# Optimization experiments

Hardware: AMD Instinct MI355X
Metric: run time of the kernel (lower is better)

Reference implementation:

```python
import jax, jax.numpy as jnp
import numpy as np

DIM, H, DH, MLP, ADIM = 512, 8, 64, 2048, 256
B, T = 4, 2048
EPS = 1e-5


def setup_inputs() -> dict:
    key = jax.random.key(0)
    ks = jax.random.split(key, 10)
    s = 0.02
    inner = H * DH
    return {
        "x": jax.random.normal(ks[0], (B, T, DIM), jnp.float32),
        "action_emb": jax.random.normal(ks[1], (B, T, ADIM), jnp.float32),
        "causal_mask": jnp.tril(jnp.ones((T, T), dtype=bool)),
        "Wqkv": jax.random.normal(ks[2], (3 * inner, DIM), jnp.float32) * s,
        "Wout": jax.random.normal(ks[3], (DIM, inner), jnp.float32) * s,
        "bout": jnp.zeros((DIM,), jnp.float32),
        "W1": jax.random.normal(ks[4], (MLP, DIM), jnp.float32) * s,
        "b1": jnp.zeros((MLP,), jnp.float32),
        "W2": jax.random.normal(ks[5], (DIM, MLP), jnp.float32) * s,
        "b2": jnp.zeros((DIM,), jnp.float32),
        # adaLN is zero-init in the module; use small random so modulation is exercised
        "Wmod": jax.random.normal(ks[6], (6 * DIM, ADIM), jnp.float32) * s,
        "bmod": jnp.zeros((6 * DIM,), jnp.float32),
    }


def _layernorm(z):
    mu = jnp.mean(z, axis=-1, keepdims=True)
    var = jnp.var(z, axis=-1, keepdims=True)
    return (z - mu) * jax.lax.rsqrt(var + EPS)


def reference(x, action_emb, causal_mask, Wqkv, Wout, bout, W1, b1, W2, b2, Wmod, bmod):
    b, t, d = x.shape
    mod = jax.nn.silu(action_emb) @ Wmod.T + bmod            # (B,T,6*dim)
    shift1, scale1, gate1, shift2, scale2, gate2 = jnp.split(mod, 6, axis=-1)

    h = _layernorm(x) * (1.0 + scale1) + shift1
    qkv = (h @ Wqkv.T).reshape(b, t, 3, H, DH)
    q, k, v = qkv[:, :, 0], qkv[:, :, 1], qkv[:, :, 2]        # (B,T,H,DH)
    scores = jnp.einsum("bqhd,bkhd->bhqk", q, k) * (DH ** -0.5)
    scores = jnp.where(causal_mask, scores, -jnp.inf)
    attn = jax.nn.softmax(scores, axis=-1)                   # dropout=eval (identity)
    h = jnp.einsum("bhqk,bkhd->bqhd", attn, v).reshape(b, t, H * DH)
    h = h @ Wout.T + bout
    x = x + gate1 * h

    h = _layernorm(x) * (1.0 + scale2) + shift2
    h = jax.nn.gelu(h @ W1.T + b1, approximate=False) @ W2.T + b2
    return x + gate2 * h
```

## Files before the change

kernel.cpp:

```cpp
#include <hip/hip_runtime.h>
#include <math.h>
#include <stdint.h>

#define BB 4
#define TT 2048
#define NTOK 8192
#define DIMD 512
#define HH 8
#define DHH 64
#define MLPD 2048
#define ADIMD 256
#define MODD 3072
#define LNEPS 1e-5f
#define LOG2E_8 0.18033688011112042f
#define PBLK 4224

typedef short short8 __attribute__((ext_vector_type(8)));
typedef unsigned short ushort4v __attribute__((ext_vector_type(4)));
typedef __bf16 bf16x8 __attribute__((ext_vector_type(8)));
typedef float f32x4 __attribute__((ext_vector_type(4)));

static __device__ __forceinline__ unsigned short f2bf(float f) {
    union { float f; unsigned u; } v; v.f = f;
    unsigned r = v.u + 0x7fffu + ((v.u >> 16) & 1u);
    return (unsigned short)(r >> 16);
}
static __device__ __forceinline__ float bf2f(unsigned short u) {
    union { unsigned u; float f; } v; v.u = (unsigned)u << 16; return v.f;
}
static __device__ __forceinline__ unsigned pk2bf(float a, float b) {
    return (unsigned)f2bf(a) | ((unsigned)f2bf(b) << 16);
}

static __device__ __forceinline__ f32x4 mfma_bf16(short8 a, short8 b, f32x4 c) {
    return __builtin_amdgcn_mfma_f32_16x16x32_bf16(
        __builtin_bit_cast(bf16x8, a), __builtin_bit_cast(bf16x8, b), c, 0, 0, 0);
}

struct CvtArgs {
    const float* s[6];
    unsigned short* d[6];
    int cum[7];
};
__global__ __launch_bounds__(256) void cvt_all(CvtArgs a)
{
    const int i = blockIdx.x * 256 + threadIdx.x;
    if (i >= a.cum[6]) return;
    int seg = 0;
    #pragma unroll
    for (int k = 1; k < 6; k++) seg += (i >= a.cum[k]);
    const int off = i - a.cum[seg];
    float4 v = ((const float4*)a.s[seg])[off];
    if (seg == 5) {
        v.x = v.x / (1.f + __expf(-v.x));
        v.y = v.y / (1.f + __expf(-v.y));
        v.z = v.z / (1.f + __expf(-v.z));
        v.w = v.w / (1.f + __expf(-v.w));
    }
    uint2 o;
    o.x = pk2bf(v.x, v.y);
    o.y = pk2bf(v.z, v.w);
    ((uint2*)a.d[seg])[off] = o;
}

template<int EPI, int BN>
__global__ __launch_bounds__(256, (BN == 128 ? 3 : 4)) void gemm_bf16(
    const unsigned short* __restrict__ A, const unsigned short* __restrict__ Bw,
    const float* __restrict__ bias, const float* __restrict__ res,
    const unsigned short* __restrict__ mod,
    int M, int N, int K,
    void* __restrict__ Cv)
{
    constexpr int MT = (BN == 128) ? 4 : 2;
    constexpr int NPB = (BN == 128) ? 4 : 2;
    __shared__ unsigned short As[128 * 76];
    __shared__ unsigned short Bs[BN * 76];

    const int tid = threadIdx.x;
    const int w = tid >> 6, lane = tid & 63;
    const int quad = lane >> 4, l16 = lane & 15;
    const int wrow = (BN == 128) ? (w >> 1) * 64 : w * 32;
    const int wcol = (BN == 128) ? (w & 1) * 64 : 0;
    const int row0 = blockIdx.y * 128, col0 = blockIdx.x * BN;

    const int srow = tid >> 3;
    const int skc  = (tid & 7) * 8;

    f32x4 acc[MT][4];
    #pragma unroll
    for (int i = 0; i < MT; i++)
        #pragma unroll
        for (int j = 0; j < 4; j++) acc[i][j] = (f32x4){0.f, 0.f, 0.f, 0.f};

    short8 pA[4], pB[NPB];
    auto prefetch = [&](int k0) {
        #pragma unroll
        for (int p = 0; p < 4; p++)
            pA[p] = *(const short8*)&A[(size_t)(row0 + srow + p * 32) * K + k0 + skc];
        #pragma unroll
        for (int p = 0; p < NPB; p++)
            pB[p] = *(const short8*)&Bw[(size_t)(col0 + srow + p * 32) * K + k0 + skc];
    };
    auto stage = [&]() {
        #pragma unroll
        for (int p = 0; p < 4; p++)
            *(short8*)&As[(srow + p * 32) * 76 + skc] = pA[p];
        #pragma unroll
        for (int p = 0; p < NPB; p++)
            *(short8*)&Bs[(srow + p * 32) * 76 + skc] = pB[p];
    };

    prefetch(0);
    stage();
    __syncthreads();

    for (int k0 = 0; k0 < K; k0 += 64) {
        const bool more = (k0 + 64 < K);
        if (more) prefetch(k0 + 64);

        #pragma unroll
        for (int ks = 0; ks < 2; ks++) {
            short8 af[MT], bf[4];
            #pragma unroll
            for (int mt = 0; mt < MT; mt++)
                af[mt] = *(const short8*)&As[(wrow + mt * 16 + l16) * 76 + ks * 32 + quad * 8];
            #pragma unroll
            for (int nt = 0; nt < 4; nt++)
                bf[nt] = *(const short8*)&Bs[(wcol + nt * 16 + l16) * 76 + ks * 32 + quad * 8];
            #pragma unroll
            for (int nt = 0; nt < 4; nt++)
                #pragma unroll
                for (int mt = 0; mt < MT; mt++)
                    acc[mt][nt] = mfma_bf16(af[mt], bf[nt], acc[mt][nt]);
        }
        __syncthreads();
        if (more) stage();
        __syncthreads();
    }

    float* Cf = (float*)Cv;
    unsigned short* Cb = (unsigned short*)Cv;
    #pragma unroll
    for (int mt = 0; mt < MT; mt++) {
        #pragma unroll
        for (int r = 0; r < 4; r++) {
            const int row = row0 + wrow + mt * 16 + quad * 4 + r;
            #pragma unroll
            for (int nt = 0; nt < 4; nt++) {
                const int col = col0 + wcol + nt * 16 + l16;
                const size_t idx = (size_t)row * N + col;
                const float v = acc[mt][nt][r];
                if (EPI == 0) {
                    Cb[idx] = f2bf(v);
                } else if (EPI == 2) {
                    float t = v + bias[col];
                    Cb[idx] = f2bf(0.5f * t * (1.f + erff(t * 0.70710678118654752f)));
                } else if (EPI == 3) {
                    float t = v + bias[col];
                    Cf[idx] = res[idx] + bf2f(mod[(size_t)row * MODD + 1024 + col]) * t;
                } else if (EPI == 4) {
                    float t = v + bias[col];
                    Cf[idx] = Cf[idx] + bf2f(mod[(size_t)row * MODD + 2560 + col]) * t;
                } else if (EPI == 5) {
                    Cb[idx] = f2bf(v + bias[col]);
                }
            }
        }
    }
}

__global__ __launch_bounds__(256) void adaln_ln(
    const float* __restrict__ src, const unsigned short* __restrict__ mod,
    unsigned short* __restrict__ dst, int shift_off, int scale_off)
{
    const int n = blockIdx.x;
    const int tid = threadIdx.x;
    const float* xr = src + (size_t)n * DIMD;
    float v0 = xr[tid], v1 = xr[tid + 256];
    float s = v0 + v1;
    float q = v0 * v0 + v1 * v1;
    #pragma unroll
    for (int o = 32; o > 0; o >>= 1) {
        s += __shfl_down(s, o);
        q += __shfl_down(q, o);
    }
    __shared__ float sh[8];
    __shared__ float mu_sh, rs_sh;
    const int wid = tid >> 6, lane = tid & 63;
    if (lane == 0) { sh[wid] = s; sh[wid + 4] = q; }
    __syncthreads();
    if (tid == 0) {
        float S = sh[0] + sh[1] + sh[2] + sh[3];
        float Q = sh[4] + sh[5] + sh[6] + sh[7];
        float mu = S * (1.f / DIMD);
        float var = Q * (1.f / DIMD) - mu * mu;
        mu_sh = mu;
        rs_sh = rsqrtf(var + LNEPS);
    }
    __syncthreads();
    const float mu = mu_sh, rs = rs_sh;
    const unsigned short* mrow = mod + (size_t)n * MODD;
    const size_t o0 = (size_t)n * DIMD + tid;
    dst[o0]       = f2bf((v0 - mu) * rs * (1.f + bf2f(mrow[scale_off + tid]))       + bf2f(mrow[shift_off + tid]));
    dst[o0 + 256] = f2bf((v1 - mu) * rs * (1.f + bf2f(mrow[scale_off + tid + 256])) + bf2f(mrow[shift_off + tid + 256]));
}

__global__ __launch_bounds__(256, 4) void attn_mfma(
    const unsigned short* __restrict__ qkv, float* __restrict__ part)
{
    __shared__ unsigned short Kt[64][76];
    __shared__ unsigned short Vt[64][76];
    __shared__ unsigned short Ps[4][16][76];

    const int f = 79 - (int)blockIdx.x;
    int qi, ch;
    if (f < 8)       { qi = f;               ch = 0; }
    else if (f < 24) { const int g = f - 8;  qi = 8 + (g >> 1);  ch = g & 1; }
    else if (f < 48) { const int g = f - 24; qi = 16 + g / 3;    ch = g % 3; }
    else             { const int g = f - 48; qi = 24 + (g >> 2); ch = g & 3; }

    const int h = blockIdx.y, b = blockIdx.z;
    const int tid = threadIdx.x;
    const int w = tid >> 6;
    const int lane = tid & 63;
    const int quad = lane >> 4;
    const int l16 = lane & 15;

    const int qw = qi * 64 + w * 16;
    const size_t tokbase = (size_t)b * TT;

    short8 qf[2];
    {
        const unsigned short* qp = qkv + (tokbase + qw + l16) * 1536 + h * 64 + quad * 8;
        #pragma unroll
        for (int hd = 0; hd < 2; hd++) {
            short8 raw = *(const short8*)(qp + hd * 32);
            short8 fr;
            #pragma unroll
            for (int j = 0; j < 8; j++)
                fr[j] = (short)f2bf(bf2f((unsigned short)raw[j]) * LOG2E_8);
            qf[hd] = fr;
        }
    }

    f32x4 Oa[4];
    float mrun = -INFINITY, lrun = 0.f;
    #pragma unroll
    for (int mt = 0; mt < 4; mt++) Oa[mt] = (f32x4){0.f, 0.f, 0.f, 0.f};

    const int k0t = ch * 8;
    const int k1t = min(k0t + 8, qi + 1);
    const int vk0 = (tid & 31) * 2;
    const int vdb = (tid >> 5) * 8;

    short8 kpre[2], vpre[2];
    auto prefetchKV = [&](int kt) {
        const unsigned short* kb = qkv + (tokbase + (size_t)kt * 64) * 1536 + 512 + h * 64;
        #pragma unroll
        for (int it = 0; it < 2; it++) {
            const int i = tid + it * 256;
            kpre[it] = *(const short8*)(kb + (size_t)(i >> 3) * 1536 + (i & 7) * 8);
        }
        const unsigned short* vb = qkv + (tokbase + (size_t)kt * 64 + vk0) * 1536 + 1024 + h * 64 + vdb;
        vpre[0] = *(const short8*)vb;
        vpre[1] = *(const short8*)(vb + 1536);
    };
    auto storeKV = [&]() {
        #pragma unroll
        for (int it = 0; it < 2; it++) {
            const int i = tid + it * 256;
            *(short8*)&Kt[i >> 3][(i & 7) * 8] = kpre[it];
        }
        #pragma unroll
        for (int j = 0; j < 8; j++) {
            *(unsigned*)&Vt[vdb + j][vk0] =
                (unsigned)(unsigned short)vpre[0][j]
                | ((unsigned)(unsigned short)vpre[1][j] << 16);
        }
    };

    prefetchKV(k0t);
    storeKV();
    __syncthreads();

    for (int kt = k0t; kt < k1t; kt++) {
        const bool haveNext = (kt + 1 < k1t);
        if (haveNext) prefetchKV(kt + 1);

        f32x4 st[4];
        #pragma unroll
        for (int mk = 0; mk < 4; mk++) {
            const short8 a0 = *(const short8*)&Kt[mk * 16 + l16][quad * 8];
            const short8 a1 = *(const short8*)&Kt[mk * 16 + l16][32 + quad * 8];
            st[mk] = (f32x4){0.f, 0.f, 0.f, 0.f};
            st[mk] = mfma_bf16(a0, qf[0], st[mk]);
            st[mk] = mfma_bf16(a1, qf[1], st[mk]);
        }
        if (kt == qi) {
            const int qrel = w * 16 + l16;
            #pragma unroll
            for (int mk = 0; mk < 4; mk++)
                #pragma unroll
                for (int r = 0; r < 4; r++)
                    if (mk * 16 + quad * 4 + r > qrel) st[mk][r] = -INFINITY;
        }
        float tm = -INFINITY;
        #pragma unroll
        for (int mk = 0; mk < 4; mk++)
            #pragma unroll
            for (int r = 0; r < 4; r++) tm = fmaxf(tm, st[mk][r]);
        tm = fmaxf(tm, __shfl_xor(tm, 16));
        tm = fmaxf(tm, __shfl_xor(tm, 32));
        const float mn = fmaxf(mrun, tm);
        const float alpha = __builtin_amdgcn_exp2f(mrun - mn);
        mrun = mn;
        float ts = 0.f;
        #pragma unroll
        for (int mk = 0; mk < 4; mk++) {
            const float p0 = __builtin_amdgcn_exp2f(st[mk][0] - mn);
            const float p1 = __builtin_amdgcn_exp2f(st[mk][1] - mn);
            const float p2 = __builtin_amdgcn_exp2f(st[mk][2] - mn);
            const float p3 = __builtin_amdgcn_exp2f(st[mk][3] - mn);
            ts += (p0 + p1) + (p2 + p3);
            const unsigned long long pk =
                (unsigned long long)pk2bf(p0, p1)
                | ((unsigned long long)pk2bf(p2, p3) << 32);
            *(unsigned long long*)&Ps[w][l16][mk * 16 + quad * 4] = pk;
        }
        ts += __shfl_xor(ts, 16);
        ts += __shfl_xor(ts, 32);
        lrun = lrun * alpha + ts;
        #pragma unroll
        for (int mt = 0; mt < 4; mt++) Oa[mt] *= alpha;
        __threadfence_block();

        short8 pf[2];
        #pragma unroll
        for (int kc = 0; kc < 2; kc++)
            pf[kc] = *(const short8*)&Ps[w][l16][kc * 32 + quad * 8];
        #pragma unroll
        for (int mt = 0; mt < 4; mt++)
            #pragma unroll
            for (int kc = 0; kc < 2; kc++) {
                const short8 vf = *(const short8*)&Vt[mt * 16 + l16][kc * 32 + quad * 8];
                Oa[mt] = mfma_bf16(vf, pf[kc], Oa[mt]);
            }

        __syncthreads();
        if (haveNext) storeKV();
        __syncthreads();
    }

    float* pO = part + ((size_t)((b * HH + h) * 80 + f)) * PBLK;
    #pragma unroll
    for (int mt = 0; mt < 4; mt++)
        *(f32x4*)&pO[(w * 16 + l16) * 64 + mt * 16 + quad * 4] = Oa[mt];
    if (quad == 0) {
        pO[4096 + (w * 16 + l16) * 2]     = mrun;
        pO[4096 + (w * 16 + l16) * 2 + 1] = lrun;
    }
}

__global__ __launch_bounds__(256) void attn_combine(
    const float* __restrict__ part, unsigned short* __restrict__ outb)
{
    const int idx = blockIdx.x * 256 + threadIdx.x;
    const int d4 = idx & 15;
    const int h = (idx >> 4) & 7;
    const int tok = idx >> 7;
    const int t = tok & (TT - 1);
    const int b = tok >> 11;
    const int qi = t >> 6;
    const int nch = (qi >> 3) + 1;
    int cum;
    if (qi < 8)       cum = qi;
    else if (qi < 16) cum = 8 + ((qi - 8) << 1);
    else if (qi < 24) cum = 24 + (qi - 16) * 3;
    else              cum = 48 + ((qi - 24) << 2);
    const int qloc = t & 63;
    const float* base = part + ((size_t)((b * HH + h) * 80 + cum)) * PBLK;

    float M = -INFINITY;
    for (int c = 0; c < nch; c++)
        M = fmaxf(M, base[c * PBLK + 4096 + qloc * 2]);
    float L = 0.f, a0 = 0.f, a1 = 0.f, a2 = 0.f, a3 = 0.f;
    for (int c = 0; c < nch; c++) {
        const float m = base[c * PBLK + 4096 + qloc * 2];
        const float l = base[c * PBLK + 4097 + qloc * 2];
        const float sc = __builtin_amdgcn_exp2f(m - M);
        L += l * sc;
        const float4 o = *(const float4*)&base[c * PBLK + qloc * 64 + d4 * 4];
        a0 += sc * o.x; a1 += sc * o.y; a2 += sc * o.z; a3 += sc * o.w;
    }
    const float inv = 1.f / L;
    const unsigned long long pk =
        (unsigned long long)pk2bf(a0 * inv, a1 * inv)
        | ((unsigned long long)pk2bf(a2 * inv, a3 * inv) << 32);
    *(unsigned long long*)&outb[(size_t)tok * DIMD + h * 64 + d4 * 4] = pk;
}

extern "C" void kernel_launch(void* const* d_in, const int* in_sizes, int n_in,
                              void* d_out, int out_size, void* d_ws, size_t ws_size,
                              hipStream_t stream)
{
    (void)in_sizes; (void)n_in; (void)out_size; (void)ws_size;

    const float* x    = (const float*)d_in[0];
    const float* aemb = (const float*)d_in[1];
    const float* Wqkv = (const float*)d_in[3];
    const float* Wout = (const float*)d_in[4];
    const float* bout = (const float*)d_in[5];
    const float* W1   = (const float*)d_in[6];
    const float* b1   = (const float*)d_in[7];
    const float* W2   = (const float*)d_in[8];
    const float* b2   = (const float*)d_in[9];
    const float* Wmod = (const float*)d_in[10];
    const float* bmod = (const float*)d_in[11];

    float* out = (float*)d_out;

    char* p = (char*)d_ws;
    unsigned short* modw = (unsigned short*)p; p += (size_t)NTOK * MODD * 2;
    unsigned short* h12  = (unsigned short*)p; p += (size_t)NTOK * DIMD * 2;
    unsigned short* qkvb = (unsigned short*)p; p += (size_t)NTOK * 1536 * 2;
    unsigned short* attw = (unsigned short*)p; p += (size_t)NTOK * DIMD * 2;
    unsigned short* hid  = qkvb;
    unsigned short* sact = (unsigned short*)p; p += (size_t)NTOK * ADIMD * 2;
    unsigned short* wq = (unsigned short*)p;   p += (size_t)1536 * 512 * 2;
    unsigned short* wo = (unsigned short*)p;   p += (size_t)512 * 512 * 2;
    unsigned short* w1 = (unsigned short*)p;   p += (size_t)2048 * 512 * 2;
    unsigned short* w2 = (unsigned short*)p;   p += (size_t)512 * 2048 * 2;
    unsigned short* wm = (unsigned short*)p;   p += (size_t)3072 * 256 * 2;
    p = (char*)(((uintptr_t)p + 255) & ~(uintptr_t)255);
    float* part = (float*)p;

    CvtArgs ca;
    ca.s[0] = Wqkv; ca.d[0] = wq;
    ca.s[1] = Wout; ca.d[1] = wo;
    ca.s[2] = W1;   ca.d[2] = w1;
    ca.s[3] = W2;   ca.d[3] = w2;
    ca.s[4] = Wmod; ca.d[4] = wm;
    ca.s[5] = aemb; ca.d[5] = sact;
    const int n4s[6] = {1536 * 512 / 4, 512 * 512 / 4, 2048 * 512 / 4,
                        512 * 2048 / 4, 3072 * 256 / 4, NTOK * ADIMD / 4};
    ca.cum[0] = 0;
    for (int i = 0; i < 6; i++) ca.cum[i + 1] = ca.cum[i] + n4s[i];
    cvt_all<<<(ca.cum[6] + 255) / 256, 256, 0, stream>>>(ca);

    gemm_bf16<5, 128><<<dim3(MODD / 128, NTOK / 128), 256, 0, stream>>>(
        sact, wm, bmod, nullptr, nullptr, NTOK, MODD, ADIMD, modw);

    adaln_ln<<<NTOK, 256, 0, stream>>>(x, modw, h12, 0, 512);

    gemm_bf16<0, 128><<<dim3(1536 / 128, NTOK / 128), 256, 0, stream>>>(
        h12, wq, nullptr, nullptr, nullptr, NTOK, 1536, DIMD, qkvb);

    attn_mfma<<<dim3(80, HH, BB), 256, 0, stream>>>(qkvb, part);
    attn_combine<<<NTOK * HH * 16 / 256, 256, 0, stream>>>(part, attw);

    gemm_bf16<3, 64><<<dim3(DIMD / 64, NTOK / 128), 256, 0, stream>>>(
        attw, wo, bout, x, modw, NTOK, DIMD, DIMD, out);

    adaln_ln<<<NTOK, 256, 0, stream>>>(out, modw, h12, 1536, 2048);

    gemm_bf16<2, 128><<<dim3(MLPD / 128, NTOK / 128), 256, 0, stream>>>(
        h12, w1, b1, nullptr, nullptr, NTOK, MLPD, DIMD, hid);

    gemm_bf16<4, 64><<<dim3(DIMD / 64, NTOK / 128), 256, 0, stream>>>(
        hid, w2, b2, nullptr, modw, NTOK, DIMD, MLPD, out);
}
```

Measured before the change: 326.6 us.

## Transpose attention probabilities via shuffles and add lazy softmax rescaling

The attention kernel no longer stages the probability tile in shared memory. It redistributes the packed bf16 values across lanes with cross-lane shuffles, which removes the LDS round trip and the block fence. Online-softmax rescaling of the running sum and output accumulator is now skipped unless some lane's new max exceeds the running max by more than 8 (log2 units), which saves the exp and multiplies in most iterations. Float-to-bf16 conversion uses the compiler's native cast, and the occupancy hint rises from 4 to 6 blocks. This risks precision drift from a stale max, and higher register pressure under the tighter launch bound.

```diff
diff --git a/kernel.cpp b/kernel.cpp
--- a/kernel.cpp
+++ b/kernel.cpp
@@ -17,13 +17,12 @@
 
 typedef short short8 __attribute__((ext_vector_type(8)));
 typedef unsigned short ushort4v __attribute__((ext_vector_type(4)));
+typedef unsigned int uint4v __attribute__((ext_vector_type(4)));
 typedef __bf16 bf16x8 __attribute__((ext_vector_type(8)));
 typedef float f32x4 __attribute__((ext_vector_type(4)));
 
 static __device__ __forceinline__ unsigned short f2bf(float f) {
-    union { float f; unsigned u; } v; v.f = f;
-    unsigned r = v.u + 0x7fffu + ((v.u >> 16) & 1u);
-    return (unsigned short)(r >> 16);
+    return __builtin_bit_cast(unsigned short, (__bf16)f);
 }
 static __device__ __forceinline__ float bf2f(unsigned short u) {
     union { unsigned u; float f; } v; v.u = (unsigned)u << 16; return v.f;
@@ -205,12 +204,11 @@
     dst[o0 + 256] = f2bf((v1 - mu) * rs * (1.f + bf2f(mrow[scale_off + tid + 256])) + bf2f(mrow[shift_off + tid + 256]));
 }
 
-__global__ __launch_bounds__(256, 4) void attn_mfma(
+__global__ __launch_bounds__(256, 6) void attn_mfma(
     const unsigned short* __restrict__ qkv, float* __restrict__ part)
 {
     __shared__ unsigned short Kt[64][76];
     __shared__ unsigned short Vt[64][76];
-    __shared__ unsigned short Ps[4][16][76];
 
     const int f = 79 - (int)blockIdx.x;
     int qi, ch;
@@ -311,33 +309,53 @@
             for (int r = 0; r < 4; r++) tm = fmaxf(tm, st[mk][r]);
         tm = fmaxf(tm, __shfl_xor(tm, 16));
         tm = fmaxf(tm, __shfl_xor(tm, 32));
-        const float mn = fmaxf(mrun, tm);
-        const float alpha = __builtin_amdgcn_exp2f(mrun - mn);
-        mrun = mn;
+        if (!__all(tm <= mrun + 8.0f)) {
+            const float mn = fmaxf(mrun, tm);
+            const float alpha = __builtin_amdgcn_exp2f(mrun - mn);
+            lrun *= alpha;
+            #pragma unroll
+            for (int mt = 0; mt < 4; mt++) Oa[mt] *= alpha;
+            mrun = mn;
+        }
         float ts = 0.f;
+        unsigned pk32[4][2];
         #pragma unroll
         for (int mk = 0; mk < 4; mk++) {
-            const float p0 = __builtin_amdgcn_exp2f(st[mk][0] - mn);
-            const float p1 = __builtin_amdgcn_exp2f(st[mk][1] - mn);
-            const float p2 = __builtin_amdgcn_exp2f(st[mk][2] - mn);
-            const float p3 = __builtin_amdgcn_exp2f(st[mk][3] - mn);
+            const float p0 = __builtin_amdgcn_exp2f(st[mk][0] - mrun);
+            const float p1 = __builtin_amdgcn_exp2f(st[mk][1] - mrun);
+            const float p2 = __builtin_amdgcn_exp2f(st[mk][2] - mrun);
+            const float p3 = __builtin_amdgcn_exp2f(st[mk][3] - mrun);
             ts += (p0 + p1) + (p2 + p3);
-            const unsigned long long pk =
-                (unsigned long long)pk2bf(p0, p1)
-                | ((unsigned long long)pk2bf(p2, p3) << 32);
-            *(unsigned long long*)&Ps[w][l16][mk * 16 + quad * 4] = pk;
+            pk32[mk][0] = pk2bf(p0, p1);
+            pk32[mk][1] = pk2bf(p2, p3);
         }
         ts += __shfl_xor(ts, 16);
         ts += __shfl_xor(ts, 32);
-        lrun = lrun * alpha + ts;
-        #pragma unroll
-        for (int mt = 0; mt < 4; mt++) Oa[mt] *= alpha;
-        __threadfence_block();
-
+        lrun += ts;
+
+        const int m_r = quad >> 1;
+        const int qbase = (quad & 1) * 32;
+        const int aA = qbase + (m_r ? 16 : 0) + l16;
+        const int aB = qbase + (m_r ? 0 : 16) + l16;
         short8 pf[2];
         #pragma unroll
-        for (int kc = 0; kc < 2; kc++)
-            pf[kc] = *(const short8*)&Ps[w][l16][kc * 32 + quad * 8];
+        for (int kc = 0; kc < 2; kc++) {
+            const unsigned vs0 = pk32[kc * 2 + (quad & 1)][0];
+            const unsigned vs1 = pk32[kc * 2 + ((quad & 1) ^ 1)][0];
+            const unsigned vs2 = pk32[kc * 2 + (quad & 1)][1];
+            const unsigned vs3 = pk32[kc * 2 + ((quad & 1) ^ 1)][1];
+            const unsigned r0 = (unsigned)__shfl((int)vs0, aA);
+            const unsigned r1 = (unsigned)__shfl((int)vs1, aB);
+            const unsigned r2 = (unsigned)__shfl((int)vs2, aA);
+            const unsigned r3 = (unsigned)__shfl((int)vs3, aB);
+            const unsigned t0 = m_r ? r1 : r0;
+            const unsigned t1 = m_r ? r3 : r2;
+            const unsigned t2 = m_r ? r0 : r1;
+            const unsigned t3 = m_r ? r2 : r3;
+            const uint4v t = (uint4v){t0, t1, t2, t3};
+            pf[kc] = __builtin_bit_cast(short8, t);
+        }
+
         #pragma unroll
         for (int mt = 0; mt < 4; mt++)
             #pragma unroll
```

Result: slower. 367.6 us (+12.6%).
